# Kernel tuning notes

Hardware: AMD Instinct MI355X
Metric: run time of the kernel (lower is better)

## Reference

```python
import jax, jax.numpy as jnp
import numpy as np

NUM_HEADS = 16
KV_CHANNELS = 128
MASK_FILL = -10000.0  # TE attention_mask_func fill value


def setup_inputs() -> dict:
    key = jax.random.key(0)
    k1, k2, k3 = jax.random.split(key, 3)
    S, B, H = 2048, 2, 2048
    hidden_states = jax.random.normal(k1, (S, B, H), dtype=jnp.float32)
    attention_mask = jnp.zeros((B, 1, S, S), dtype=bool)  # True = masked out
    qkv_weight = jax.random.normal(k2, (H, 3 * H), dtype=jnp.float32) * (1.0 / np.sqrt(H))
    qkv_bias = jnp.zeros((3 * H,), dtype=jnp.float32)
    proj_weight = jax.random.normal(k3, (H, H), dtype=jnp.float32) * (1.0 / np.sqrt(H))
    proj_bias = jnp.zeros((H,), dtype=jnp.float32)
    return {
        "hidden_states": hidden_states,
        "attention_mask": attention_mask,
        "qkv_weight": qkv_weight,
        "qkv_bias": qkv_bias,
        "proj_weight": proj_weight,
        "proj_bias": proj_bias,
    }


def reference(hidden_states, attention_mask, qkv_weight, qkv_bias, proj_weight, proj_bias):
    S, B, H = hidden_states.shape
    nh, d = NUM_HEADS, KV_CHANNELS
    # QKV GEMM: [s,b,H] @ [H,3H] -> [s,b,3H] -> [s,b,nh,3d] -> split
    mixed = hidden_states @ qkv_weight + qkv_bias
    mixed = mixed.reshape(S, B, nh, 3 * d)
    q, k, v = jnp.split(mixed, 3, axis=-1)  # each [s,b,nh,d]
    # BMM1 with 1/sqrt(d) scaling (layer_number=None -> no layer scaling)
    norm_factor = jnp.asarray(np.sqrt(d), dtype=hidden_states.dtype)
    scores = jnp.einsum("sbhd,tbhd->bhst", q, k) / norm_factor  # [b,nh,s,s]
    # causal mask (future positions masked) OR'd with provided bool padding mask
    causal = ~jnp.tril(jnp.ones((S, S), dtype=bool))  # True above diagonal
    mask = jnp.logical_or(causal[None, None], attention_mask)
    scores = jnp.where(mask, jnp.asarray(MASK_FILL, scores.dtype), scores)
    probs = jax.nn.softmax(scores, axis=-1)
    # dropout is identity in eval mode (training=False)
    # BMM2: [b,nh,s,t] x [t,b,nh,d] -> [s,b,nh,d] -> [s,b,H]
    context = jnp.einsum("bhst,tbhd->sbhd", probs, v).reshape(S, B, H)
    # output projection; TE Dense(use_bias=False, return_bias=True) returns bias
    out = context @ proj_weight
    return out, proj_bias
```

## Files before the change

### kernel.cpp

```cpp
#include <hip/hip_runtime.h>
#include <cstdint>
#include <math.h>

#define S_LEN 2048
#define BATCH 2
#define HID   2048
#define NHEAD 16
#define DHEAD 128

typedef _Float16 h8 __attribute__((ext_vector_type(8)));
typedef _Float16 h4 __attribute__((ext_vector_type(4)));
typedef float f32x4 __attribute__((ext_vector_type(4)));

__device__ __forceinline__ void gload16(const void* g, void* l) {
  __builtin_amdgcn_global_load_lds(
      (const __attribute__((address_space(1))) unsigned int*)g,
      (__attribute__((address_space(3))) unsigned int*)l, 16, 0, 0);
}

template <bool HAS_BIAS, bool OUT_HALF>
__global__ __launch_bounds__(512) void gemm_256(
    const _Float16* __restrict__ A, const _Float16* __restrict__ Bt,
    const float* __restrict__ bias, void* __restrict__ Cout, int M, int N,
    int K) {
  __shared__ _Float16 LA[2][2][8192];
  __shared__ _Float16 LB[2][2][8192];
  const int tid = (int)threadIdx.x;
  const int wave = tid >> 6, lane = tid & 63;
  const int ln = lane & 15, quad = lane >> 4;
  const int wm = wave >> 2, wn = wave & 3;
  const int bm = (int)blockIdx.y * 256, bn = (int)blockIdx.x * 256;
  const int NT = K >> 6;

  const int rA = wave * 16 + (lane >> 3);
  const int gc8 = ((lane & 7) ^ (lane >> 3)) * 8;
  const uint32_t oA00 = (uint32_t)(bm + rA) * (uint32_t)K + (uint32_t)gc8;
  const uint32_t oA01 = oA00 + (uint32_t)(8 * K);
  const uint32_t oA10 = oA00 + (uint32_t)(128 * K);
  const uint32_t oA11 = oA10 + (uint32_t)(8 * K);
  const uint32_t oB00 = (uint32_t)(bn + rA) * (uint32_t)K + (uint32_t)gc8;
  const uint32_t oB01 = oB00 + (uint32_t)(8 * K);
  const uint32_t oB10 = oB00 + (uint32_t)(128 * K);
  const uint32_t oB11 = oB10 + (uint32_t)(8 * K);
  const int cw0 = wave * 1024;
  const int cw1 = cw0 + 512;

#define STAGE_A(h_, bb_, u_)                                           \
  {                                                                    \
    gload16(A + (oA##h_##0 + (uint32_t)(u_)*64u), &LA[bb_][h_][cw0]);  \
    gload16(A + (oA##h_##1 + (uint32_t)(u_)*64u), &LA[bb_][h_][cw1]);  \
  }
#define STAGE_B(h_, bb_, u_)                                           \
  {                                                                    \
    gload16(Bt + (oB##h_##0 + (uint32_t)(u_)*64u), &LB[bb_][h_][cw0]); \
    gload16(Bt + (oB##h_##1 + (uint32_t)(u_)*64u), &LB[bb_][h_][cw1]); \
  }

  const int arow = ln * 64;
  const int sc0 = ((quad ^ (ln & 7))) * 8;
  const int sc1 = (((4 + quad) ^ (ln & 7))) * 8;
  const int bro = (wn & 1) * 4096;

  f32x4 acc[8][4];
#pragma unroll
  for (int m = 0; m < 8; m++)
#pragma unroll
    for (int n = 0; n < 4; n++) acc[m][n] = (f32x4){0.f, 0.f, 0.f, 0.f};
  h8 aLo[4][2], aHi[4][2], bF[4][2];

#define QUAD(aF_, mo_, no_)                                                  \
  _Pragma("unroll") for (int mm_ = 0; mm_ < 4; mm_++)                        \
      _Pragma("unroll") for (int nn_ = 0; nn_ < 2; nn_++) {                  \
    acc[(mo_) + mm_][(no_) + nn_] = __builtin_amdgcn_mfma_f32_16x16x32_f16(  \
        aF_[mm_][0], bF[(no_) + nn_][0], acc[(mo_) + mm_][(no_) + nn_], 0,   \
        0, 0);                                                               \
    acc[(mo_) + mm_][(no_) + nn_] = __builtin_amdgcn_mfma_f32_16x16x32_f16(  \
        aF_[mm_][1], bF[(no_) + nn_][1], acc[(mo_) + mm_][(no_) + nn_], 0,   \
        0, 0);                                                               \
  }

  STAGE_A(0, 0, 0) STAGE_A(1, 0, 0) STAGE_B(0, 0, 0) STAGE_B(1, 0, 0)
  STAGE_A(0, 1, 1) STAGE_B(0, 1, 1) STAGE_B(1, 1, 1)
  asm volatile("s_waitcnt vmcnt(6)" ::: "memory");
  __builtin_amdgcn_s_barrier();
#pragma unroll
  for (int n = 0; n < 2; n++) {
    bF[n][0] = *(const h8*)&LB[0][wn >> 1][bro + n * 1024 + arow + sc0];
    bF[n][1] = *(const h8*)&LB[0][wn >> 1][bro + n * 1024 + arow + sc1];
  }

  for (int u = 0; u < NT; ++u) {
    const int bb = u & 1;

#pragma unroll
    for (int m = 0; m < 4; m++) {
      aLo[m][0] = *(const h8*)&LA[bb][wm][m * 1024 + arow + sc0];
      aLo[m][1] = *(const h8*)&LA[bb][wm][m * 1024 + arow + sc1];
    }
    if (u + 1 < NT) STAGE_A(1, bb ^ 1, u + 1)
    __builtin_amdgcn_s_barrier();
    if (u) {
      __builtin_amdgcn_s_setprio(1);
      QUAD(aHi, 4, 2)
      __builtin_amdgcn_s_setprio(0);
    }
    __builtin_amdgcn_s_barrier();

#pragma unroll
    for (int m = 0; m < 4; m++) {
      aHi[m][0] = *(const h8*)&LA[bb][wm][(m + 4) * 1024 + arow + sc0];
      aHi[m][1] = *(const h8*)&LA[bb][wm][(m + 4) * 1024 + arow + sc1];
    }
    __builtin_amdgcn_s_barrier();
    __builtin_amdgcn_s_setprio(1);
    QUAD(aLo, 0, 0)
    __builtin_amdgcn_s_setprio(0);
    __builtin_amdgcn_s_barrier();

#pragma unroll
    for (int n = 2; n < 4; n++) {
      bF[n][0] = *(const h8*)&LB[bb][wn >> 1][bro + n * 1024 + arow + sc0];
      bF[n][1] = *(const h8*)&LB[bb][wn >> 1][bro + n * 1024 + arow + sc1];
    }
    if (u + 2 < NT) STAGE_A(0, bb, u + 2)
    __builtin_amdgcn_s_barrier();
    __builtin_amdgcn_s_setprio(1);
    QUAD(aHi, 4, 0)
    __builtin_amdgcn_s_setprio(0);
    __builtin_amdgcn_s_barrier();

    if (u + 2 < NT) {
      STAGE_B(0, bb, u + 2) STAGE_B(1, bb, u + 2)
      asm volatile("s_waitcnt vmcnt(6)" ::: "memory");
    } else if (u + 1 < NT) {
      asm volatile("s_waitcnt vmcnt(0)" ::: "memory");
    }
    __builtin_amdgcn_s_barrier();
    if (u + 1 < NT) {
      const int nbb = bb ^ 1;
#pragma unroll
      for (int n = 0; n < 2; n++) {
        bF[n][0] = *(const h8*)&LB[nbb][wn >> 1][bro + n * 1024 + arow + sc0];
        bF[n][1] = *(const h8*)&LB[nbb][wn >> 1][bro + n * 1024 + arow + sc1];
      }
    }
    __builtin_amdgcn_s_setprio(1);
    QUAD(aLo, 0, 2)
    __builtin_amdgcn_s_setprio(0);
    __builtin_amdgcn_s_barrier();
  }

  __builtin_amdgcn_s_setprio(1);
  QUAD(aHi, 4, 2)
  __builtin_amdgcn_s_setprio(0);
#undef QUAD
#undef STAGE_A
#undef STAGE_B

#pragma unroll
  for (int m = 0; m < 8; m++) {
#pragma unroll
    for (int r = 0; r < 4; r++) {
      const size_t row = (size_t)(bm + wm * 128 + m * 16 + quad * 4 + r);
#pragma unroll
      for (int n = 0; n < 4; n++) {
        const int col = bn + wn * 64 + n * 16 + ln;
        float v = acc[m][n][r];
        if (HAS_BIAS) v += bias[col];
        if (OUT_HALF)
          ((_Float16*)Cout)[row * N + col] = (_Float16)v;
        else
          ((float*)Cout)[row * N + col] = v;
      }
    }
  }
}

template <bool HAS_BIAS, bool OUT_HALF>
__global__ __launch_bounds__(512) void gemm_128(
    const _Float16* __restrict__ A, const _Float16* __restrict__ Bt,
    const float* __restrict__ bias, void* __restrict__ Cout, int M, int N,
    int K) {
  __shared__ _Float16 LA[2][8192];
  __shared__ _Float16 LB[2][16384];
  const int tid = (int)threadIdx.x;
  const int wave = tid >> 6, lane = tid & 63;
  const int ln = lane & 15, quad = lane >> 4;
  const int wm = wave >> 2, wn = wave & 3;
  const int bm = (int)blockIdx.y * 128, bn = (int)blockIdx.x * 256;
  const int NT = K >> 6;

  const int gc8 = ((lane & 7) ^ (lane >> 3)) * 8;
  const uint32_t oA0 =
      (uint32_t)(bm + wave * 8 + (lane >> 3)) * (uint32_t)K + (uint32_t)gc8;
  const uint32_t oA1 = oA0 + (uint32_t)(64 * K);
  const uint32_t oB00 =
      (uint32_t)(bn + wave * 16 + (lane >> 3)) * (uint32_t)K + (uint32_t)gc8;
  const uint32_t oB01 = oB00 + (uint32_t)(8 * K);
  const uint32_t oB10 = oB00 + (uint32_t)(128 * K);
  const uint32_t oB11 = oB10 + (uint32_t)(8 * K);

#define STAGE128(bb_, u_)                                                    \
  {                                                                          \
    gload16(A + (oA0 + (uint32_t)(u_)*64u), &LA[bb_][wave * 512]);           \
    gload16(A + (oA1 + (uint32_t)(u_)*64u), &LA[bb_][4096 + wave * 512]);    \
    gload16(Bt + (oB00 + (uint32_t)(u_)*64u), &LB[bb_][wave * 1024]);        \
    gload16(Bt + (oB01 + (uint32_t)(u_)*64u), &LB[bb_][wave * 1024 + 512]);  \
    gload16(Bt + (oB10 + (uint32_t)(u_)*64u), &LB[bb_][8192 + wave * 1024]); \
    gload16(Bt + (oB11 + (uint32_t)(u_)*64u),                                \
            &LB[bb_][8192 + wave * 1024 + 512]);                             \
  }

  const int arow = ln * 64;
  const int sc0 = ((quad ^ (ln & 7))) * 8;
  const int sc1 = (((4 + quad) ^ (ln & 7))) * 8;
  const int abase = wm * 4096;
  const int bbase = wn * 4096;

  f32x4 acc[4][4];
#pragma unroll
  for (int m = 0; m < 4; m++)
#pragma unroll
    for (int n = 0; n < 4; n++) acc[m][n] = (f32x4){0.f, 0.f, 0.f, 0.f};
  h8 aF[4][2], bF[4][2];

#define HQUAD(n0_)                                                           \
  _Pragma("unroll") for (int mm_ = 0; mm_ < 4; mm_++)                        \
      _Pragma("unroll") for (int nn_ = 0; nn_ < 2; nn_++) {                  \
    acc[mm_][(n0_) + nn_] = __builtin_amdgcn_mfma_f32_16x16x32_f16(          \
        aF[mm_][0], bF[(n0_) + nn_][0], acc[mm_][(n0_) + nn_], 0, 0, 0);     \
    acc[mm_][(n0_) + nn_] = __builtin_amdgcn_mfma_f32_16x16x32_f16(          \
        aF[mm_][1], bF[(n0_) + nn_][1], acc[mm_][(n0_) + nn_], 0, 0, 0);     \
  }

  STAGE128(0, 0)
  STAGE128(1, 1)
  asm volatile("s_waitcnt vmcnt(6)" ::: "memory");
  __builtin_amdgcn_s_barrier();

  for (int u = 0; u < NT; ++u) {
    const int bb = u & 1;

#pragma unroll
    for (int m = 0; m < 4; m++) {
      aF[m][0] = *(const h8*)&LA[bb][abase + m * 1024 + arow + sc0];
      aF[m][1] = *(const h8*)&LA[bb][abase + m * 1024 + arow + sc1];
    }
#pragma unroll
    for (int n = 0; n < 2; n++) {
      bF[n][0] = *(const h8*)&LB[bb][bbase + n * 1024 + arow + sc0];
      bF[n][1] = *(const h8*)&LB[bb][bbase + n * 1024 + arow + sc1];
    }
    __builtin_amdgcn_s_barrier();
    __builtin_amdgcn_s_setprio(1);
    HQUAD(0)
    __builtin_amdgcn_s_setprio(0);
    __builtin_amdgcn_s_barrier();

#pragma unroll
    for (int n = 2; n < 4; n++) {
      bF[n][0] = *(const h8*)&LB[bb][bbase + n * 1024 + arow + sc0];
      bF[n][1] = *(const h8*)&LB[bb][bbase + n * 1024 + arow + sc1];
    }
    if (u + 2 < NT) {
      STAGE128(bb, u + 2)
      asm volatile("s_waitcnt vmcnt(6)" ::: "memory");
    } else if (u + 1 < NT) {
      asm volatile("s_waitcnt vmcnt(0)" ::: "memory");
    }
    __builtin_amdgcn_s_barrier();
    __builtin_amdgcn_s_setprio(1);
    HQUAD(2)
    __builtin_amdgcn_s_setprio(0);
    __builtin_amdgcn_s_barrier();
  }
#undef HQUAD
#undef STAGE128

#pragma unroll
  for (int m = 0; m < 4; m++) {
#pragma unroll
    for (int r = 0; r < 4; r++) {
      const size_t row = (size_t)(bm + wm * 64 + m * 16 + quad * 4 + r);
#pragma unroll
      for (int n = 0; n < 4; n++) {
        const int col = bn + wn * 64 + n * 16 + ln;
        float v = acc[m][n][r];
        if (HAS_BIAS) v += bias[col];
        if (OUT_HALF)
          ((_Float16*)Cout)[row * N + col] = (_Float16)v;
        else
          ((float*)Cout)[row * N + col] = v;
      }
    }
  }
}

__global__ __launch_bounds__(256) void transpose_cvt(
    const float* __restrict__ in, _Float16* __restrict__ out, int K, int N) {
  __shared__ float t[64][65];
  const int bn = blockIdx.x * 64, bk = blockIdx.y * 64;
  const int tid = (int)threadIdx.x;
  {
    const int r0 = tid >> 4, c4 = (tid & 15) * 4;
#pragma unroll
    for (int i = 0; i < 4; i++) {
      const int r = r0 + 16 * i;
      float4 v = *(const float4*)&in[(size_t)(bk + r) * N + bn + c4];
      t[r][c4] = v.x;
      t[r][c4 + 1] = v.y;
      t[r][c4 + 2] = v.z;
      t[r][c4 + 3] = v.w;
    }
  }
  __syncthreads();
  {
    const int c0 = tid >> 4, r4 = (tid & 15) * 4;
#pragma unroll
    for (int i = 0; i < 4; i++) {
      const int c = c0 + 16 * i;
      h4 o = {(_Float16)t[r4][c], (_Float16)t[r4 + 1][c],
              (_Float16)t[r4 + 2][c], (_Float16)t[r4 + 3][c]};
      *(h4*)&out[(size_t)(bn + c) * K + bk + r4] = o;
    }
  }
}

__global__ __launch_bounds__(256) void cvt_fp16(const float* __restrict__ in,
                                                _Float16* __restrict__ out,
                                                int n4) {
  int i = blockIdx.x * blockDim.x + threadIdx.x;
  if (i < n4) {
    float4 v = ((const float4*)in)[i];
    h4 o = {(_Float16)v.x, (_Float16)v.y, (_Float16)v.z, (_Float16)v.w};
    *(h4*)&out[4 * (size_t)i] = o;
  }
}

__global__ __launch_bounds__(256) void pack_kv(
    const _Float16* __restrict__ mixed, _Float16* __restrict__ KP,
    _Float16* __restrict__ VP) {
  __shared__ _Float16 Tv[128 * 40];
  const int kt = blockIdx.x;
  const int z = blockIdx.y;
  const int kb = kt * 32;
  const int tid = threadIdx.x;
  const size_t RS = (size_t)BATCH * NHEAD * 384;
  const _Float16* base = mixed + (size_t)z * 384;

  {
    const int r = tid >> 3, d0 = (tid & 7) * 16;
    const _Float16* src = base + (size_t)(kb + r) * RS + 256 + d0;
    h8 v0 = *(const h8*)src;
    h8 v1 = *(const h8*)(src + 8);
#pragma unroll
    for (int e = 0; e < 8; e++) Tv[(d0 + e) * 40 + r] = v0[e];
#pragma unroll
    for (int e = 0; e < 8; e++) Tv[(d0 + 8 + e) * 40 + r] = v1[e];
  }
  __syncthreads();

  const size_t tb = ((size_t)z * 64 + kt) * 8 * 512;
#pragma unroll
  for (int c = 0; c < 2; c++) {
    const int idx = tid + 256 * c;
    const int i = idx >> 6, l = idx & 63;
    const int ln = l & 15, quad = l >> 4;
    {
      const int jn = i >> 2, kq = i & 3;
      h8 v = *(const h8*)(base + (size_t)(kb + 16 * jn + ln) * RS + 128 +
                          32 * kq + 8 * quad);
      *(h8*)&KP[tb + (size_t)i * 512 + l * 8] = v;
    }
    {
      h8 v = *(const h8*)&Tv[(16 * i + ln) * 40 + 8 * quad];
      *(h8*)&VP[tb + (size_t)i * 512 + l * 8] = v;
    }
  }
}

__global__ __launch_bounds__(256) void flash_attn_v7(
    const _Float16* __restrict__ mixed, const _Float16* __restrict__ KP,
    const _Float16* __restrict__ VP, const unsigned char* __restrict__ mask,
    _Float16* __restrict__ ctx) {
  const int qt = (int)gridDim.x - 1 - (int)blockIdx.x;
  const int h = blockIdx.y, b = blockIdx.z;
  const int z = b * NHEAD + h;
  const int qb = qt * 64;
  const int tid = threadIdx.x;
  const int wave = tid >> 6, lane = tid & 63;
  const int ln = lane & 15, quad = lane >> 4;

  __shared__ _Float16 Kbuf[2][8 * 512];
  __shared__ _Float16 Vbuf[2][8 * 512];
  __shared__ _Float16 St[4][16 * 40];

  const size_t RS = (size_t)BATCH * NHEAD * 384;
  const _Float16* base = mixed + (size_t)z * 384;
  const unsigned char* mbase = mask + (size_t)b * S_LEN * S_LEN;
  const float scale = 0.08838834764831845f;

  h8 qfrag[4];
  {
    const size_t row = (size_t)(qb + 16 * wave + ln);
#pragma unroll
    for (int kq = 0; kq < 4; kq++) {
      h8 v = *(const h8*)(base + row * RS + 32 * kq + 8 * quad);
#pragma unroll
      for (int j = 0; j < 8; j++) v[j] = (_Float16)((float)v[j] * scale);
      qfrag[kq] = v;
    }
  }

  f32x4 o[8];
#pragma unroll
  for (int nt = 0; nt < 8; nt++) o[nt] = (f32x4){0.f, 0.f, 0.f, 0.f};
  float lpart[4] = {0.f, 0.f, 0.f, 0.f};

  const int ntiles = 2 * qt + 2;

  const size_t zt = (size_t)z * 64;
#define STAGE(kt_, buf_)                                                   \
  {                                                                        \
    const size_t tbk = (zt + (kt_)) * (8 * 512) + lane * 8;                \
    _Pragma("unroll") for (int c = 0; c < 2; c++) {                        \
      const int ch = 2 * wave + c;                                         \
      gload16(KP + tbk + ch * 512, &Kbuf[buf_][ch * 512]);                 \
      gload16(VP + tbk + ch * 512, &Vbuf[buf_][ch * 512]);                 \
    }                                                                      \
  }

  STAGE(0, 0)

  for (int kt = 0; kt < ntiles; kt++) {
    const int kb = kt * 32;
    const int cur = kt & 1;
    __syncthreads();

    if (kt + 1 < ntiles) STAGE(kt + 1, cur ^ 1)

    unsigned char mreg[4][2];
#pragma unroll
    for (int r = 0; r < 4; r++)
#pragma unroll
      for (int jn = 0; jn < 2; jn++)
        mreg[r][jn] = mbase[(size_t)(qb + 16 * wave + 4 * quad + r) * S_LEN +
                            kb + 16 * jn + ln];

    f32x4 s[2];
    s[0] = (f32x4){0.f, 0.f, 0.f, 0.f};
    s[1] = (f32x4){0.f, 0.f, 0.f, 0.f};
#pragma unroll
    for (int kq = 0; kq < 4; kq++) {
#pragma unroll
      for (int jn = 0; jn < 2; jn++) {
        h8 bk = *(const h8*)&Kbuf[cur][(jn * 4 + kq) * 512 + lane * 8];
        s[jn] = __builtin_amdgcn_mfma_f32_16x16x32_f16(qfrag[kq], bk, s[jn], 0,
                                                       0, 0);
      }
    }

#pragma unroll
    for (int jn = 0; jn < 2; jn++)
#pragma unroll
      for (int r = 0; r < 4; r++) {
        const int grow = qb + 16 * wave + 4 * quad + r;
        const int gcol = kb + 16 * jn + ln;
        const float sv = ((gcol > grow) || mreg[r][jn]) ? -10000.0f : s[jn][r];
        const float p = __expf(sv);
        lpart[r] += p;
        St[wave][(4 * quad + r) * 40 + 16 * jn + ln] = (_Float16)p;
      }
    __threadfence_block();

    {
      h8 ap = *(const h8*)&St[wave][ln * 40 + 8 * quad];
#pragma unroll
      for (int nt = 0; nt < 8; nt++) {
        h8 bv = *(const h8*)&Vbuf[cur][nt * 512 + lane * 8];
        o[nt] = __builtin_amdgcn_mfma_f32_16x16x32_f16(ap, bv, o[nt], 0, 0, 0);
      }
    }
  }
#undef STAGE

#pragma unroll
  for (int r = 0; r < 4; r++) {
    float l = lpart[r];
#pragma unroll
    for (int off = 8; off >= 1; off >>= 1) l += __shfl_xor(l, off, 16);
    const float inv_l = 1.0f / l;
    const size_t row_g = (size_t)(qb + 16 * wave + 4 * quad + r);
    _Float16* dst = ctx + (row_g * BATCH + b) * HID + h * DHEAD;
#pragma unroll
    for (int nt = 0; nt < 8; nt++)
      dst[16 * nt + ln] = (_Float16)(o[nt][r] * inv_l);
  }
}

__global__ void copy_bias(const float* __restrict__ src,
                          float* __restrict__ dst) {
  int i = blockIdx.x * blockDim.x + threadIdx.x;
  if (i < HID) dst[i] = src[i];
}

extern "C" void kernel_launch(void* const* d_in, const int* in_sizes, int n_in,
                              void* d_out, int out_size, void* d_ws,
                              size_t ws_size, hipStream_t stream) {
  (void)in_sizes;
  (void)n_in;
  const float* hs = (const float*)d_in[0];
  const unsigned char* mask = (const unsigned char*)d_in[1];
  const float* qkv_w = (const float*)d_in[2];
  const float* qkv_b = (const float*)d_in[3];
  const float* proj_w = (const float*)d_in[4];
  const float* proj_b = (const float*)d_in[5];
  float* out = (float*)d_out;

  const size_t M = (size_t)S_LEN * BATCH;
  const size_t mixed_e = M * 3 * HID;
  const size_t qkvwt_e = (size_t)3 * HID * HID;
  const size_t hsh_e = M * HID;
  const size_t projwt_e = (size_t)HID * HID;
  const size_t ctx_e = M * HID;
  const size_t need =
      (mixed_e + qkvwt_e + hsh_e + projwt_e + ctx_e) * sizeof(_Float16);
  if (ws_size < need) return;

  _Float16* mixed = (_Float16*)d_ws;
  _Float16* qkv_wt = mixed + mixed_e;
  _Float16* hs_h = qkv_wt + qkvwt_e;
  _Float16* proj_wt = hs_h + hsh_e;
  _Float16* ctx = proj_wt + projwt_e;
  _Float16* KP = hs_h;
  _Float16* VP = qkv_wt;

  cvt_fp16<<<(int)(hsh_e / 4 / 256), 256, 0, stream>>>(hs, hs_h,
                                                       (int)(hsh_e / 4));
  transpose_cvt<<<dim3(3 * HID / 64, HID / 64), 256, 0, stream>>>(
      qkv_w, qkv_wt, HID, 3 * HID);
  transpose_cvt<<<dim3(HID / 64, HID / 64), 256, 0, stream>>>(
      proj_w, proj_wt, HID, HID);

  gemm_256<true, true><<<dim3(3 * HID / 256, M / 256), 512, 0, stream>>>(
      hs_h, qkv_wt, qkv_b, mixed, (int)M, 3 * HID, HID);

  pack_kv<<<dim3(S_LEN / 32, BATCH * NHEAD), 256, 0, stream>>>(mixed, KP, VP);

  flash_attn_v7<<<dim3(S_LEN / 64, NHEAD, BATCH), 256, 0, stream>>>(
      mixed, KP, VP, mask, ctx);

  gemm_128<false, false><<<dim3(HID / 256, M / 128), 512, 0, stream>>>(
      ctx, proj_wt, nullptr, out, (int)M, HID, HID);

  copy_bias<<<(HID + 255) / 256, 256, 0, stream>>>(proj_b, out + M * HID);
}
```

Before: 448.0 us.

## Pack mask into causal-merged bitmask and use 128-row GEMM for QKV

Adds a pre-pass that packs the byte attention mask together with the causal mask into one 32-bit bitmask per 32 columns, stored temporarily in the output buffer. The attention kernel then reads one word per row per tile instead of eight bytes per lane, and needs no per-element causal compare. The QKV projection also switches from the 256x256-tile GEMM to the 128x256 variant, whose grid has more blocks. The cost is an extra kernel launch and a full pass over the byte mask. The smaller GEMM tile may also lose data reuse.

Measured after the change: 447.2 us. Within noise of the previous version (-0.2%).

```diff
diff --git a/kernel.cpp b/kernel.cpp
--- a/kernel.cpp
+++ b/kernel.cpp
@@ -16,164 +16,6 @@
   __builtin_amdgcn_global_load_lds(
       (const __attribute__((address_space(1))) unsigned int*)g,
       (__attribute__((address_space(3))) unsigned int*)l, 16, 0, 0);
-}
-
-template <bool HAS_BIAS, bool OUT_HALF>
-__global__ __launch_bounds__(512) void gemm_256(
-    const _Float16* __restrict__ A, const _Float16* __restrict__ Bt,
-    const float* __restrict__ bias, void* __restrict__ Cout, int M, int N,
-    int K) {
-  __shared__ _Float16 LA[2][2][8192];
-  __shared__ _Float16 LB[2][2][8192];
-  const int tid = (int)threadIdx.x;
-  const int wave = tid >> 6, lane = tid & 63;
-  const int ln = lane & 15, quad = lane >> 4;
-  const int wm = wave >> 2, wn = wave & 3;
-  const int bm = (int)blockIdx.y * 256, bn = (int)blockIdx.x * 256;
-  const int NT = K >> 6;
-
-  const int rA = wave * 16 + (lane >> 3);
-  const int gc8 = ((lane & 7) ^ (lane >> 3)) * 8;
-  const uint32_t oA00 = (uint32_t)(bm + rA) * (uint32_t)K + (uint32_t)gc8;
-  const uint32_t oA01 = oA00 + (uint32_t)(8 * K);
-  const uint32_t oA10 = oA00 + (uint32_t)(128 * K);
-  const uint32_t oA11 = oA10 + (uint32_t)(8 * K);
-  const uint32_t oB00 = (uint32_t)(bn + rA) * (uint32_t)K + (uint32_t)gc8;
-  const uint32_t oB01 = oB00 + (uint32_t)(8 * K);
-  const uint32_t oB10 = oB00 + (uint32_t)(128 * K);
-  const uint32_t oB11 = oB10 + (uint32_t)(8 * K);
-  const int cw0 = wave * 1024;
-  const int cw1 = cw0 + 512;
-
-#define STAGE_A(h_, bb_, u_)                                           \
-  {                                                                    \
-    gload16(A + (oA##h_##0 + (uint32_t)(u_)*64u), &LA[bb_][h_][cw0]);  \
-    gload16(A + (oA##h_##1 + (uint32_t)(u_)*64u), &LA[bb_][h_][cw1]);  \
-  }
-#define STAGE_B(h_, bb_, u_)                                           \
-  {                                                                    \
-    gload16(Bt + (oB##h_##0 + (uint32_t)(u_)*64u), &LB[bb_][h_][cw0]); \
-    gload16(Bt + (oB##h_##1 + (uint32_t)(u_)*64u), &LB[bb_][h_][cw1]); \
-  }
-
-  const int arow = ln * 64;
-  const int sc0 = ((quad ^ (ln & 7))) * 8;
-  const int sc1 = (((4 + quad) ^ (ln & 7))) * 8;
-  const int bro = (wn & 1) * 4096;
-
-  f32x4 acc[8][4];
-#pragma unroll
-  for (int m = 0; m < 8; m++)
-#pragma unroll
-    for (int n = 0; n < 4; n++) acc[m][n] = (f32x4){0.f, 0.f, 0.f, 0.f};
-  h8 aLo[4][2], aHi[4][2], bF[4][2];
-
-#define QUAD(aF_, mo_, no_)                                                  \
-  _Pragma("unroll") for (int mm_ = 0; mm_ < 4; mm_++)                        \
-      _Pragma("unroll") for (int nn_ = 0; nn_ < 2; nn_++) {                  \
-    acc[(mo_) + mm_][(no_) + nn_] = __builtin_amdgcn_mfma_f32_16x16x32_f16(  \
-        aF_[mm_][0], bF[(no_) + nn_][0], acc[(mo_) + mm_][(no_) + nn_], 0,   \
-        0, 0);                                                               \
-    acc[(mo_) + mm_][(no_) + nn_] = __builtin_amdgcn_mfma_f32_16x16x32_f16(  \
-        aF_[mm_][1], bF[(no_) + nn_][1], acc[(mo_) + mm_][(no_) + nn_], 0,   \
-        0, 0);                                                               \
-  }
-
-  STAGE_A(0, 0, 0) STAGE_A(1, 0, 0) STAGE_B(0, 0, 0) STAGE_B(1, 0, 0)
-  STAGE_A(0, 1, 1) STAGE_B(0, 1, 1) STAGE_B(1, 1, 1)
-  asm volatile("s_waitcnt vmcnt(6)" ::: "memory");
-  __builtin_amdgcn_s_barrier();
-#pragma unroll
-  for (int n = 0; n < 2; n++) {
-    bF[n][0] = *(const h8*)&LB[0][wn >> 1][bro + n * 1024 + arow + sc0];
-    bF[n][1] = *(const h8*)&LB[0][wn >> 1][bro + n * 1024 + arow + sc1];
-  }
-
-  for (int u = 0; u < NT; ++u) {
-    const int bb = u & 1;
-
-#pragma unroll
-    for (int m = 0; m < 4; m++) {
-      aLo[m][0] = *(const h8*)&LA[bb][wm][m * 1024 + arow + sc0];
-      aLo[m][1] = *(const h8*)&LA[bb][wm][m * 1024 + arow + sc1];
-    }
-    if (u + 1 < NT) STAGE_A(1, bb ^ 1, u + 1)
-    __builtin_amdgcn_s_barrier();
-    if (u) {
-      __builtin_amdgcn_s_setprio(1);
-      QUAD(aHi, 4, 2)
-      __builtin_amdgcn_s_setprio(0);
-    }
-    __builtin_amdgcn_s_barrier();
-
-#pragma unroll
-    for (int m = 0; m < 4; m++) {
-      aHi[m][0] = *(const h8*)&LA[bb][wm][(m + 4) * 1024 + arow + sc0];
-      aHi[m][1] = *(const h8*)&LA[bb][wm][(m + 4) * 1024 + arow + sc1];
-    }
-    __builtin_amdgcn_s_barrier();
-    __builtin_amdgcn_s_setprio(1);
-    QUAD(aLo, 0, 0)
-    __builtin_amdgcn_s_setprio(0);
-    __builtin_amdgcn_s_barrier();
-
-#pragma unroll
-    for (int n = 2; n < 4; n++) {
-      bF[n][0] = *(const h8*)&LB[bb][wn >> 1][bro + n * 1024 + arow + sc0];
-      bF[n][1] = *(const h8*)&LB[bb][wn >> 1][bro + n * 1024 + arow + sc1];
-    }
-    if (u + 2 < NT) STAGE_A(0, bb, u + 2)
-    __builtin_amdgcn_s_barrier();
-    __builtin_amdgcn_s_setprio(1);
-    QUAD(aHi, 4, 0)
-    __builtin_amdgcn_s_setprio(0);
-    __builtin_amdgcn_s_barrier();
-
-    if (u + 2 < NT) {
-      STAGE_B(0, bb, u + 2) STAGE_B(1, bb, u + 2)
-      asm volatile("s_waitcnt vmcnt(6)" ::: "memory");
-    } else if (u + 1 < NT) {
-      asm volatile("s_waitcnt vmcnt(0)" ::: "memory");
-    }
-    __builtin_amdgcn_s_barrier();
-    if (u + 1 < NT) {
-      const int nbb = bb ^ 1;
-#pragma unroll
-      for (int n = 0; n < 2; n++) {
-        bF[n][0] = *(const h8*)&LB[nbb][wn >> 1][bro + n * 1024 + arow + sc0];
-        bF[n][1] = *(const h8*)&LB[nbb][wn >> 1][bro + n * 1024 + arow + sc1];
-      }
-    }
-    __builtin_amdgcn_s_setprio(1);
-    QUAD(aLo, 0, 2)
-    __builtin_amdgcn_s_setprio(0);
-    __builtin_amdgcn_s_barrier();
-  }
-
-  __builtin_amdgcn_s_setprio(1);
-  QUAD(aHi, 4, 2)
-  __builtin_amdgcn_s_setprio(0);
-#undef QUAD
-#undef STAGE_A
-#undef STAGE_B
-
-#pragma unroll
-  for (int m = 0; m < 8; m++) {
-#pragma unroll
-    for (int r = 0; r < 4; r++) {
-      const size_t row = (size_t)(bm + wm * 128 + m * 16 + quad * 4 + r);
-#pragma unroll
-      for (int n = 0; n < 4; n++) {
-        const int col = bn + wn * 64 + n * 16 + ln;
-        float v = acc[m][n][r];
-        if (HAS_BIAS) v += bias[col];
-        if (OUT_HALF)
-          ((_Float16*)Cout)[row * N + col] = (_Float16)v;
-        else
-          ((float*)Cout)[row * N + col] = v;
-      }
-    }
-  }
 }
 
 template <bool HAS_BIAS, bool OUT_HALF>
@@ -337,6 +179,33 @@
   }
 }
 
+__global__ __launch_bounds__(256) void pack_mask(
+    const unsigned char* __restrict__ m, uint32_t* __restrict__ pm) {
+  const int i = blockIdx.x * 256 + threadIdx.x;
+  const int w = i & 63, r = (i >> 6) & (S_LEN - 1), b = i >> 17;
+  const uint32_t* src =
+      (const uint32_t*)(m + ((size_t)b * S_LEN + r) * S_LEN + w * 32);
+  uint32_t bits = 0;
+#pragma unroll
+  for (int k = 0; k < 8; k++) {
+    const uint32_t v = src[k];
+    bits |= ((v & 0x000000FFu) ? 1u : 0u) << (4 * k);
+    bits |= ((v & 0x0000FF00u) ? 1u : 0u) << (4 * k + 1);
+    bits |= ((v & 0x00FF0000u) ? 1u : 0u) << (4 * k + 2);
+    bits |= ((v & 0xFF000000u) ? 1u : 0u) << (4 * k + 3);
+  }
+  const int c0 = w * 32;
+  uint32_t caus;
+  if (c0 > r) {
+    caus = 0xFFFFFFFFu;
+  } else if (r - c0 >= 31) {
+    caus = 0u;
+  } else {
+    caus = ~((2u << (r - c0)) - 1u);
+  }
+  pm[i] = bits | caus;
+}
+
 __global__ __launch_bounds__(256) void pack_kv(
     const _Float16* __restrict__ mixed, _Float16* __restrict__ KP,
     _Float16* __restrict__ VP) {
@@ -379,9 +248,9 @@
   }
 }
 
-__global__ __launch_bounds__(256) void flash_attn_v7(
+__global__ __launch_bounds__(256) void flash_attn_v8(
     const _Float16* __restrict__ mixed, const _Float16* __restrict__ KP,
-    const _Float16* __restrict__ VP, const unsigned char* __restrict__ mask,
+    const _Float16* __restrict__ VP, const uint32_t* __restrict__ pmask,
     _Float16* __restrict__ ctx) {
   const int qt = (int)gridDim.x - 1 - (int)blockIdx.x;
   const int h = blockIdx.y, b = blockIdx.z;
@@ -397,7 +266,7 @@
 
   const size_t RS = (size_t)BATCH * NHEAD * 384;
   const _Float16* base = mixed + (size_t)z * 384;
-  const unsigned char* mbase = mask + (size_t)b * S_LEN * S_LEN;
+  const uint32_t* pmb = pmask + (size_t)b * S_LEN * 64;
   const float scale = 0.08838834764831845f;
 
   h8 qfrag[4];
@@ -432,20 +301,17 @@
 
   STAGE(0, 0)
 
+  const uint32_t* pmr = pmb + (size_t)(qb + 16 * wave + 4 * quad) * 64;
+
   for (int kt = 0; kt < ntiles; kt++) {
-    const int kb = kt * 32;
     const int cur = kt & 1;
     __syncthreads();
 
     if (kt + 1 < ntiles) STAGE(kt + 1, cur ^ 1)
 
-    unsigned char mreg[4][2];
-#pragma unroll
-    for (int r = 0; r < 4; r++)
-#pragma unroll
-      for (int jn = 0; jn < 2; jn++)
-        mreg[r][jn] = mbase[(size_t)(qb + 16 * wave + 4 * quad + r) * S_LEN +
-                            kb + 16 * jn + ln];
+    uint32_t mw[4];
+#pragma unroll
+    for (int r = 0; r < 4; r++) mw[r] = pmr[(size_t)r * 64 + kt];
 
     f32x4 s[2];
     s[0] = (f32x4){0.f, 0.f, 0.f, 0.f};
@@ -461,16 +327,16 @@
     }
 
 #pragma unroll
-    for (int jn = 0; jn < 2; jn++)
-#pragma unroll
-      for (int r = 0; r < 4; r++) {
-        const int grow = qb + 16 * wave + 4 * quad + r;
-        const int gcol = kb + 16 * jn + ln;
-        const float sv = ((gcol > grow) || mreg[r][jn]) ? -10000.0f : s[jn][r];
+    for (int r = 0; r < 4; r++) {
+      const uint32_t ms = mw[r] >> ln;
+#pragma unroll
+      for (int jn = 0; jn < 2; jn++) {
+        const float sv = ((ms >> (16 * jn)) & 1u) ? -10000.0f : s[jn][r];
         const float p = __expf(sv);
         lpart[r] += p;
         St[wave][(4 * quad + r) * 40 + 16 * jn + ln] = (_Float16)p;
       }
+    }
     __threadfence_block();
 
     {
@@ -534,6 +400,7 @@
   _Float16* ctx = proj_wt + projwt_e;
   _Float16* KP = hs_h;
   _Float16* VP = qkv_wt;
+  uint32_t* pmask = (uint32_t*)out;
 
   cvt_fp16<<<(int)(hsh_e / 4 / 256), 256, 0, stream>>>(hs, hs_h,
                                                        (int)(hsh_e / 4));
@@ -541,14 +408,15 @@
       qkv_w, qkv_wt, HID, 3 * HID);
   transpose_cvt<<<dim3(HID / 64, HID / 64), 256, 0, stream>>>(
       proj_w, proj_wt, HID, HID);
-
-  gemm_256<true, true><<<dim3(3 * HID / 256, M / 256), 512, 0, stream>>>(
+  pack_mask<<<(BATCH * S_LEN * 64) / 256, 256, 0, stream>>>(mask, pmask);
+
+  gemm_128<true, true><<<dim3(3 * HID / 256, M / 128), 512, 0, stream>>>(
       hs_h, qkv_wt, qkv_b, mixed, (int)M, 3 * HID, HID);
 
   pack_kv<<<dim3(S_LEN / 32, BATCH * NHEAD), 256, 0, stream>>>(mixed, KP, VP);
 
-  flash_attn_v7<<<dim3(S_LEN / 64, NHEAD, BATCH), 256, 0, stream>>>(
-      mixed, KP, VP, mask, ctx);
+  flash_attn_v8<<<dim3(S_LEN / 64, NHEAD, BATCH), 256, 0, stream>>>(
+      mixed, KP, VP, pmask, ctx);
 
   gemm_128<false, false><<<dim3(HID / 256, M / 128), 512, 0, stream>>>(
       ctx, proj_wt, nullptr, out, (int)M, HID, HID);
```
